# Optimization experiments

Hardware: AMD Instinct MI355X
Metric: run time of the kernel (lower is better)

The kernel has to match this reference:

```python
import jax, jax.numpy as jnp
import numpy as np

DT = 0.01
MAXLAG = 3.0
NLAG = int(MAXLAG / DT)   # same float->int math as the torch module
NMA = 20


def setup_inputs() -> dict:
    key = jax.random.key(0)
    k1, k2, k3, k4 = jax.random.split(key, 4)
    B, C, F = 32, 128, 2049  # F = nfast/2 + 1, nfast = 4096
    data1 = jax.random.normal(k1, (B, C, F, 2), dtype=jnp.float32)
    data2 = jax.random.normal(k2, (B, C, F, 2), dtype=jnp.float32)
    event1 = jax.random.randint(k3, (B,), 0, 100000, dtype=jnp.int64 if jax.config.jax_enable_x64 else jnp.int32)
    event2 = jax.random.randint(k4, (B,), 0, 100000, dtype=jnp.int64 if jax.config.jax_enable_x64 else jnp.int32)
    return {"data1": data1, "data2": data2, "event1": event1, "event2": event2}


def reference(data1, data2, event1, event2):
    # view_as_complex: trailing dim 2 = (re, im)
    c1 = jax.lax.complex(data1[..., 0], data1[..., 1])  # [B, C, F]
    c2 = jax.lax.complex(data2[..., 0], data2[..., 1])
    F = c1.shape[-1]
    nfast = (F - 1) * 2

    # cross-spectrum and inverse rFFT (channel_shift == 0)
    xf = jnp.conj(c1) * c2
    xt = jnp.fft.irfft(xf, n=nfast, axis=-1)          # [B, C, nfast]
    xt = jnp.roll(xt, nfast // 2, axis=-1)
    xcor = xt[..., nfast // 2 - NLAG + 1: nfast // 2 + NLAG]  # [B, C, T], T = 2*NLAG-1

    # AvgPool1d(NMA, stride=1, padding=NMA//2) over the CHANNEL axis (dim 1),
    # count_include_pad=True -> windowed zero-padded sum divided by NMA, keep first C rows
    pad = NMA // 2
    C = xcor.shape[1]
    wsum = jax.lax.reduce_window(
        xcor, 0.0, jax.lax.add,
        window_dimensions=(1, NMA, 1), window_strides=(1, 1, 1),
        padding=[(0, 0), (pad, pad), (0, 0)])          # [B, C+1, T]
    xcor = (wsum / NMA)[:, :C, :]                      # [B, C, T]

    # peak pick: pick max, but swap in min where |min| > max
    vmax = jnp.max(xcor, axis=-1)
    imax = jnp.argmax(xcor, axis=-1)
    vmin = jnp.min(xcor, axis=-1)
    imin = jnp.argmin(xcor, axis=-1)
    ineg = jnp.abs(vmin) > vmax
    cc = jnp.where(ineg, vmin, vmax)                   # [B, C]
    idx = jnp.where(ineg, imin, imax)
    tshift = (idx - NLAG + 1).astype(jnp.float32) * DT # [B, C]
    return (cc, tshift, event1, event2)
```

## Files before the change

### kernel.cpp

```cpp
#include <hip/hip_runtime.h>
#include <math.h>

#define NBINS 2049
#define NXC   599
#define LST   640
#define TWO_PI 6.283185307179586f

#define CPAD(c) ((c) + 2 * ((c) >> 6))

struct cpx { float r, i; };
__device__ inline cpx cmul(cpx a, cpx b) { return cpx{a.r * b.r - a.i * b.i, a.r * b.i + a.i * b.r}; }

__device__ inline void dft4i(float& r0, float& i0, float& r1, float& i1,
                             float& r2, float& i2, float& r3, float& i3) {
    float t0r = r0 + r2, t0i = i0 + i2;
    float t1r = r0 - r2, t1i = i0 - i2;
    float t2r = r1 + r3, t2i = i1 + i3;
    float t3r = r1 - r3, t3i = i1 - i3;
    r0 = t0r + t2r; i0 = t0i + t2i;
    r2 = t0r - t2r; i2 = t0i - t2i;
    r1 = t1r - t3i; i1 = t1i + t3r;
    r3 = t1r + t3i; i3 = t1i - t3r;
}

__device__ inline void radix8_bfly(float r[8], float im[8]) {
    float er0 = r[0], ei0 = im[0], er1 = r[2], ei1 = im[2];
    float er2 = r[4], ei2 = im[4], er3 = r[6], ei3 = im[6];
    float or0 = r[1], oi0 = im[1], or1 = r[3], oi1 = im[3];
    float or2 = r[5], oi2 = im[5], or3 = r[7], oi3 = im[7];
    dft4i(er0, ei0, er1, ei1, er2, ei2, er3, ei3);
    dft4i(or0, oi0, or1, oi1, or2, oi2, or3, oi3);
    const float C = 0.70710678118654752f;
    float w1r = C * (or1 - oi1), w1i = C * (or1 + oi1);
    float w2r = -oi2,            w2i = or2;
    float w3r = -C * (or3 + oi3), w3i = C * (or3 - oi3);
    r[0] = er0 + or0; im[0] = ei0 + oi0;
    r[4] = er0 - or0; im[4] = ei0 - oi0;
    r[1] = er1 + w1r; im[1] = ei1 + w1i;
    r[5] = er1 - w1r; im[5] = ei1 - w1i;
    r[2] = er2 + w2r; im[2] = ei2 + w2i;
    r[6] = er2 - w2r; im[6] = ei2 - w2i;
    r[3] = er3 + w3r; im[3] = ei3 + w3i;
    r[7] = er3 - w3r; im[7] = ei3 - w3i;
}

__device__ inline void dft16i(float xr[16], float xi[16]) {
    float er[8], ei[8], odr[8], odi[8];
#pragma unroll
    for (int k = 0; k < 8; ++k) {
        er[k] = xr[2 * k];      ei[k] = xi[2 * k];
        odr[k] = xr[2 * k + 1]; odi[k] = xi[2 * k + 1];
    }
    radix8_bfly(er, ei);
    radix8_bfly(odr, odi);
    const float c1 = 0.92387953251128675613f;
    const float s1 = 0.38268343236508977173f;
    const float C  = 0.70710678118654752440f;
    float tr[8], td[8];
    tr[0] = odr[0];                      td[0] = odi[0];
    tr[1] = c1 * odr[1] - s1 * odi[1];   td[1] = c1 * odi[1] + s1 * odr[1];
    tr[2] = C * (odr[2] - odi[2]);       td[2] = C * (odr[2] + odi[2]);
    tr[3] = s1 * odr[3] - c1 * odi[3];   td[3] = s1 * odi[3] + c1 * odr[3];
    tr[4] = -odi[4];                     td[4] = odr[4];
    tr[5] = -s1 * odr[5] - c1 * odi[5];  td[5] = -s1 * odi[5] + c1 * odr[5];
    tr[6] = -C * (odr[6] + odi[6]);      td[6] = C * (odr[6] - odi[6]);
    tr[7] = -c1 * odr[7] - s1 * odi[7];  td[7] = -c1 * odi[7] + s1 * odr[7];
#pragma unroll
    for (int k = 0; k < 8; ++k) {
        xr[k]     = er[k] + tr[k];  xi[k]     = ei[k] + td[k];
        xr[k + 8] = er[k] - tr[k];  xi[k + 8] = ei[k] - td[k];
    }
}

__device__ inline void apply_tw15(float zr[16], float zi[16], float cs, float sn) {
    cpx w[16];
    w[1]  = cpx{cs, sn};
    w[2]  = cmul(w[1], w[1]);
    w[3]  = cmul(w[1], w[2]);
    w[4]  = cmul(w[2], w[2]);
    w[5]  = cmul(w[2], w[3]);
    w[6]  = cmul(w[3], w[3]);
    w[7]  = cmul(w[3], w[4]);
    w[8]  = cmul(w[4], w[4]);
    w[9]  = cmul(w[4], w[5]);
    w[10] = cmul(w[5], w[5]);
    w[11] = cmul(w[5], w[6]);
    w[12] = cmul(w[6], w[6]);
    w[13] = cmul(w[6], w[7]);
    w[14] = cmul(w[7], w[7]);
    w[15] = cmul(w[7], w[8]);
#pragma unroll
    for (int k = 1; k < 16; ++k) {
        float a = zr[k] * w[k].r - zi[k] * w[k].i;
        float b = zr[k] * w[k].i + zi[k] * w[k].r;
        zr[k] = a; zi[k] = b;
    }
}

__global__ __launch_bounds__(256, 4) void k1_fft(const float2* __restrict__ d1,
                                                 const float2* __restrict__ d2,
                                                 float* __restrict__ ws) {
    __shared__ float2 S[2][2112];
    const int g = threadIdx.x >> 7;
    const int tt = threadIdx.x & 127;
    const int row = (blockIdx.x << 1) | g;
    float2* Sg = S[g];
    const float2* p1 = d1 + (long)row * NBINS;
    const float2* p2 = d2 + (long)row * NBINS;

    float zr[16], zi[16];
    float sn, cs;

    const float WC[16] = { 1.0f, 0.98078528040323044913f, 0.92387953251128675613f,
        0.83146961230254523708f, 0.70710678118654752440f, 0.55557023301960222474f,
        0.38268343236508977173f, 0.19509032201612826785f, 0.0f,
        -0.19509032201612826785f, -0.38268343236508977173f, -0.55557023301960222474f,
        -0.70710678118654752440f, -0.83146961230254523708f, -0.92387953251128675613f,
        -0.98078528040323044913f };
    const float WS[16] = { 0.0f, 0.19509032201612826785f, 0.38268343236508977173f,
        0.55557023301960222474f, 0.70710678118654752440f, 0.83146961230254523708f,
        0.92387953251128675613f, 0.98078528040323044913f, 1.0f,
        0.98078528040323044913f, 0.92387953251128675613f, 0.83146961230254523708f,
        0.70710678118654752440f, 0.55557023301960222474f, 0.38268343236508977173f,
        0.19509032201612826785f };
    __sincosf((float)tt * (TWO_PI / 4096.0f), &sn, &cs);
#pragma unroll
    for (int j = 0; j < 16; ++j) {
        int c = tt + 128 * j;
        int mc = 2048 - c;
        float2 a = p1[c],  bb = p2[c];
        float2 am = p1[mc], bm = p2[mc];
        float xr = a.x * bb.x + a.y * bb.y;
        float xi = a.x * bb.y - a.y * bb.x;
        float yr2 = am.x * bm.x + am.y * bm.y;
        float yi2 = am.x * bm.y - am.y * bm.x;
        if (c == 0) { xi = 0.0f; yi2 = 0.0f; }
        float er = 0.5f * (xr + yr2), ei = 0.5f * (xi - yi2);
        float dr = 0.5f * (xr - yr2), di = 0.5f * (xi + yi2);
        float twr = cs * WC[j] - sn * WS[j];
        float twi = cs * WS[j] + sn * WC[j];
        zr[j] = er - twi * dr - twr * di;
        zi[j] = ei + twr * dr - twi * di;
    }

    dft16i(zr, zi);
    __sincosf((float)tt * (TWO_PI / 2048.0f), &sn, &cs);
    apply_tw15(zr, zi, cs, sn);
#pragma unroll
    for (int k = 0; k < 16; ++k)
        Sg[CPAD(tt + 128 * k)] = make_float2(zr[k], zi[k]);

    __syncthreads();

    const int s2 = tt >> 3, i2 = tt & 7;
    const int base2 = 128 * s2 + i2;
#pragma unroll
    for (int j = 0; j < 16; ++j) {
        float2 v = Sg[CPAD(base2 + 8 * j)];
        zr[j] = v.x; zi[j] = v.y;
    }
    dft16i(zr, zi);
    __sincosf((float)i2 * (TWO_PI / 128.0f), &sn, &cs);
    apply_tw15(zr, zi, cs, sn);
#pragma unroll
    for (int k = 0; k < 16; ++k)
        Sg[CPAD(base2 + 8 * k)] = make_float2(zr[k], zi[k]);

    __syncthreads();

    float ar[8], ai[8], br[8], bi[8];
#pragma unroll
    for (int r = 0; r < 4; ++r) {
        float4 v = *(const float4*)&Sg[CPAD(16 * tt + 2 * r)];
        ar[2 * r] = v.x; ai[2 * r] = v.y; ar[2 * r + 1] = v.z; ai[2 * r + 1] = v.w;
    }
#pragma unroll
    for (int r = 0; r < 4; ++r) {
        float4 v = *(const float4*)&Sg[CPAD(16 * tt + 8 + 2 * r)];
        br[2 * r] = v.x; bi[2 * r] = v.y; br[2 * r + 1] = v.z; bi[2 * r + 1] = v.w;
    }
    radix8_bfly(ar, ai);
    radix8_bfly(br, bi);

    const float sc = 1.0f / 2048.0f;
    float* wrow = ws + (long)row * LST;
    {
        int sb = 2 * tt;
        int m0 = (sb >> 4) + 16 * (sb & 15);
        if (m0 <= 149) { wrow[2 * m0 + 299] = ar[0] * sc; wrow[2 * m0 + 300] = ai[0] * sc; }
        if (m0 >= 107)      { wrow[2 * m0 - 213] = ar[7] * sc; wrow[2 * m0 - 212] = ai[7] * sc; }
        else if (m0 == 106) { wrow[0] = ai[7] * sc; }
    }
    {
        int sb = 2 * tt + 1;
        int m0 = (sb >> 4) + 16 * (sb & 15);
        if (m0 <= 149) { wrow[2 * m0 + 299] = br[0] * sc; wrow[2 * m0 + 300] = bi[0] * sc; }
        if (m0 >= 107)      { wrow[2 * m0 - 213] = br[7] * sc; wrow[2 * m0 - 212] = bi[7] * sc; }
        else if (m0 == 106) { wrow[0] = bi[7] * sc; }
    }
}

__global__ __launch_bounds__(640) void k2a_prefix(float* __restrict__ ws) {
    const int b = blockIdx.x;
    const int l = threadIdx.x;
    if (l >= NXC) return;
    float* base = ws + (long)b * 128 * LST + l;
    float run = 0.0f;
#pragma unroll 4
    for (int c = 0; c < 128; ++c) {
        run += base[c * LST];
        base[c * LST] = run;
    }
}

__global__ __launch_bounds__(128) void k2b_pick(const float* __restrict__ ws,
                                                const int* __restrict__ e1,
                                                const int* __restrict__ e2,
                                                float* __restrict__ out) {
    const int bc = blockIdx.x;
    const int b = bc >> 7, c = bc & 127;
    const int t = threadIdx.x;
    const float* Pb = ws + (long)(b * 128) * LST;
    const float* hi = Pb + (long)min(c + 9, 127) * LST;
    const bool has_lo = (c >= 11);
    const float* lo = Pb + (long)(has_lo ? (c - 11) : 0) * LST;

    float vmax = -3.0e38f; int imax = 0;
    float vmin = 3.0e38f;  int imin = 0;
    for (int l = t; l < NXC; l += 128) {
        float s = hi[l] - (has_lo ? lo[l] : 0.0f);
        s *= (1.0f / 20.0f);
        if (s > vmax) { vmax = s; imax = l; }
        if (s < vmin) { vmin = s; imin = l; }
    }

    __shared__ float smax[128], smin[128];
    __shared__ int   sxi[128], sni[128];
    smax[t] = vmax; sxi[t] = imax; smin[t] = vmin; sni[t] = imin;
    __syncthreads();
    for (int off = 64; off > 0; off >>= 1) {
        if (t < off) {
            float v2 = smax[t + off]; int i2 = sxi[t + off];
            if (v2 > smax[t] || (v2 == smax[t] && i2 < sxi[t])) { smax[t] = v2; sxi[t] = i2; }
            float u2 = smin[t + off]; int j2 = sni[t + off];
            if (u2 < smin[t] || (u2 == smin[t] && j2 < sni[t])) { smin[t] = u2; sni[t] = j2; }
        }
        __syncthreads();
    }
    if (t == 0) {
        float vx = smax[0], vn = smin[0];
        int ix = sxi[0], in_ = sni[0];
        bool ineg = fabsf(vn) > vx;
        float ccv = ineg ? vn : vx;
        int idx = ineg ? in_ : ix;
        out[bc] = ccv;
        out[4096 + bc] = (float)(idx - 299) * 0.01f;
    }
    if (bc == 0 && t < 32) out[8192 + t] = (float)e1[t];
    if (bc == 1 && t < 32) out[8224 + t] = (float)e2[t];
}

extern "C" void kernel_launch(void* const* d_in, const int* in_sizes, int n_in,
                              void* d_out, int out_size, void* d_ws, size_t ws_size,
                              hipStream_t stream) {
    const float2* d1 = (const float2*)d_in[0];
    const float2* d2 = (const float2*)d_in[1];
    const int* e1 = (const int*)d_in[2];
    const int* e2 = (const int*)d_in[3];
    float* out = (float*)d_out;
    float* ws = (float*)d_ws;

    k1_fft<<<dim3(2048), dim3(256), 0, stream>>>(d1, d2, ws);
    k2a_prefix<<<dim3(32), dim3(640), 0, stream>>>(ws);
    k2b_pick<<<dim3(4096), dim3(128), 0, stream>>>(ws, e1, e2, out);
}
```

Measured before the change: 57.39 us.

## Stage cross-spectrum in LDS to halve global loads and split prefix-scan blocks

The FFT kernel now computes each cross-spectrum bin once, stores it in shared memory, and reads the mirrored bin from LDS instead of reloading both inputs from global memory. This halves global traffic. The 1/2048 scale is folded into the pre-twiddle factor, and each block now handles one row with 128 threads. The prefix-scan kernel is split from 32 blocks of 640 threads into 160 blocks of 128 threads to spread across more CUs. An extra barrier and the LDS round trip are added in exchange.

```diff
diff --git a/kernel.cpp b/kernel.cpp
--- a/kernel.cpp
+++ b/kernel.cpp
@@ -97,19 +97,30 @@
     }
 }
 
-__global__ __launch_bounds__(256, 4) void k1_fft(const float2* __restrict__ d1,
+__global__ __launch_bounds__(128, 4) void k1_fft(const float2* __restrict__ d1,
                                                  const float2* __restrict__ d2,
                                                  float* __restrict__ ws) {
-    __shared__ float2 S[2][2112];
-    const int g = threadIdx.x >> 7;
-    const int tt = threadIdx.x & 127;
-    const int row = (blockIdx.x << 1) | g;
-    float2* Sg = S[g];
+    __shared__ float2 S[2113];
+    const int row = blockIdx.x;
+    const int tt = threadIdx.x;
     const float2* p1 = d1 + (long)row * NBINS;
     const float2* p2 = d2 + (long)row * NBINS;
 
-    float zr[16], zi[16];
-    float sn, cs;
+    float xr_[16], xi_[16];
+#pragma unroll
+    for (int j = 0; j < 16; ++j) {
+        int c = tt + 128 * j;
+        float2 a = p1[c], bb = p2[c];
+        xr_[j] = a.x * bb.x + a.y * bb.y;
+        xi_[j] = a.x * bb.y - a.y * bb.x;
+        S[CPAD(c)] = make_float2(xr_[j], xi_[j]);
+    }
+    if (tt == 127) {
+        float2 a = p1[2048], bb = p2[2048];
+        S[2112] = make_float2(a.x * bb.x + a.y * bb.y, 0.0f);
+    }
+    if (tt == 0) xi_[0] = 0.0f;
+    __syncthreads();
 
     const float WC[16] = { 1.0f, 0.98078528040323044913f, 0.92387953251128675613f,
         0.83146961230254523708f, 0.70710678118654752440f, 0.55557023301960222474f,
@@ -123,20 +134,15 @@
         0.98078528040323044913f, 0.92387953251128675613f, 0.83146961230254523708f,
         0.70710678118654752440f, 0.55557023301960222474f, 0.38268343236508977173f,
         0.19509032201612826785f };
+    float zr[16], zi[16];
+    float sn, cs;
     __sincosf((float)tt * (TWO_PI / 4096.0f), &sn, &cs);
+    const float h = 2.44140625e-4f;
 #pragma unroll
     for (int j = 0; j < 16; ++j) {
-        int c = tt + 128 * j;
-        int mc = 2048 - c;
-        float2 a = p1[c],  bb = p2[c];
-        float2 am = p1[mc], bm = p2[mc];
-        float xr = a.x * bb.x + a.y * bb.y;
-        float xi = a.x * bb.y - a.y * bb.x;
-        float yr2 = am.x * bm.x + am.y * bm.y;
-        float yi2 = am.x * bm.y - am.y * bm.x;
-        if (c == 0) { xi = 0.0f; yi2 = 0.0f; }
-        float er = 0.5f * (xr + yr2), ei = 0.5f * (xi - yi2);
-        float dr = 0.5f * (xr - yr2), di = 0.5f * (xi + yi2);
+        float2 m = S[CPAD(2048 - tt - 128 * j)];
+        float er = h * (xr_[j] + m.x), ei = h * (xi_[j] - m.y);
+        float dr = h * (xr_[j] - m.x), di = h * (xi_[j] + m.y);
         float twr = cs * WC[j] - sn * WS[j];
         float twi = cs * WS[j] + sn * WC[j];
         zr[j] = er - twi * dr - twr * di;
@@ -146,17 +152,17 @@
     dft16i(zr, zi);
     __sincosf((float)tt * (TWO_PI / 2048.0f), &sn, &cs);
     apply_tw15(zr, zi, cs, sn);
+    __syncthreads();
 #pragma unroll
     for (int k = 0; k < 16; ++k)
-        Sg[CPAD(tt + 128 * k)] = make_float2(zr[k], zi[k]);
-
+        S[CPAD(tt + 128 * k)] = make_float2(zr[k], zi[k]);
     __syncthreads();
 
     const int s2 = tt >> 3, i2 = tt & 7;
     const int base2 = 128 * s2 + i2;
 #pragma unroll
     for (int j = 0; j < 16; ++j) {
-        float2 v = Sg[CPAD(base2 + 8 * j)];
+        float2 v = S[CPAD(base2 + 8 * j)];
         zr[j] = v.x; zi[j] = v.y;
     }
     dft16i(zr, zi);
@@ -164,45 +170,43 @@
     apply_tw15(zr, zi, cs, sn);
 #pragma unroll
     for (int k = 0; k < 16; ++k)
-        Sg[CPAD(base2 + 8 * k)] = make_float2(zr[k], zi[k]);
-
+        S[CPAD(base2 + 8 * k)] = make_float2(zr[k], zi[k]);
     __syncthreads();
 
     float ar[8], ai[8], br[8], bi[8];
 #pragma unroll
     for (int r = 0; r < 4; ++r) {
-        float4 v = *(const float4*)&Sg[CPAD(16 * tt + 2 * r)];
+        float4 v = *(const float4*)&S[CPAD(16 * tt + 2 * r)];
         ar[2 * r] = v.x; ai[2 * r] = v.y; ar[2 * r + 1] = v.z; ai[2 * r + 1] = v.w;
     }
 #pragma unroll
     for (int r = 0; r < 4; ++r) {
-        float4 v = *(const float4*)&Sg[CPAD(16 * tt + 8 + 2 * r)];
+        float4 v = *(const float4*)&S[CPAD(16 * tt + 8 + 2 * r)];
         br[2 * r] = v.x; bi[2 * r] = v.y; br[2 * r + 1] = v.z; bi[2 * r + 1] = v.w;
     }
     radix8_bfly(ar, ai);
     radix8_bfly(br, bi);
 
-    const float sc = 1.0f / 2048.0f;
     float* wrow = ws + (long)row * LST;
     {
         int sb = 2 * tt;
         int m0 = (sb >> 4) + 16 * (sb & 15);
-        if (m0 <= 149) { wrow[2 * m0 + 299] = ar[0] * sc; wrow[2 * m0 + 300] = ai[0] * sc; }
-        if (m0 >= 107)      { wrow[2 * m0 - 213] = ar[7] * sc; wrow[2 * m0 - 212] = ai[7] * sc; }
-        else if (m0 == 106) { wrow[0] = ai[7] * sc; }
+        if (m0 <= 149) { wrow[2 * m0 + 299] = ar[0]; wrow[2 * m0 + 300] = ai[0]; }
+        if (m0 >= 107)      { wrow[2 * m0 - 213] = ar[7]; wrow[2 * m0 - 212] = ai[7]; }
+        else if (m0 == 106) { wrow[0] = ai[7]; }
     }
     {
         int sb = 2 * tt + 1;
         int m0 = (sb >> 4) + 16 * (sb & 15);
-        if (m0 <= 149) { wrow[2 * m0 + 299] = br[0] * sc; wrow[2 * m0 + 300] = bi[0] * sc; }
-        if (m0 >= 107)      { wrow[2 * m0 - 213] = br[7] * sc; wrow[2 * m0 - 212] = bi[7] * sc; }
-        else if (m0 == 106) { wrow[0] = bi[7] * sc; }
-    }
-}
-
-__global__ __launch_bounds__(640) void k2a_prefix(float* __restrict__ ws) {
-    const int b = blockIdx.x;
-    const int l = threadIdx.x;
+        if (m0 <= 149) { wrow[2 * m0 + 299] = br[0]; wrow[2 * m0 + 300] = bi[0]; }
+        if (m0 >= 107)      { wrow[2 * m0 - 213] = br[7]; wrow[2 * m0 - 212] = bi[7]; }
+        else if (m0 == 106) { wrow[0] = bi[7]; }
+    }
+}
+
+__global__ __launch_bounds__(128) void k2a_prefix(float* __restrict__ ws) {
+    const int b = blockIdx.x / 5;
+    const int l = (blockIdx.x % 5) * 128 + threadIdx.x;
     if (l >= NXC) return;
     float* base = ws + (long)b * 128 * LST + l;
     float run = 0.0f;
@@ -270,7 +274,7 @@
     float* out = (float*)d_out;
     float* ws = (float*)d_ws;
 
-    k1_fft<<<dim3(2048), dim3(256), 0, stream>>>(d1, d2, ws);
-    k2a_prefix<<<dim3(32), dim3(640), 0, stream>>>(ws);
+    k1_fft<<<dim3(4096), dim3(128), 0, stream>>>(d1, d2, ws);
+    k2a_prefix<<<dim3(160), dim3(128), 0, stream>>>(ws);
     k2b_pick<<<dim3(4096), dim3(128), 0, stream>>>(ws, e1, e2, out);
 }
```

Measured after the change: 50.16 us. -12.6%, faster.
